# Kernel tuning notes

Measured on AMD Instinct MI355X. Metric: run time of the kernel, lower is better.

The kernel has to match this reference:

```python
import jax, jax.numpy as jnp
import numpy as np

ALPHA = 1.5
TEMPERATURE = 1.0
N_ITER = 25
N_EMBED = 2048
NUM_EXPERTS = 64
N_TOKENS = 32768


def entmax_bisect(X, alpha=ALPHA, n_iter=N_ITER):
    """Faithful port of entmax.entmax_bisect forward (dim=-1)."""
    d = X.shape[-1]
    inv = 1.0 / (alpha - 1.0)
    Xa = X * (alpha - 1.0)
    max_val = jnp.max(Xa, axis=-1, keepdims=True)
    # _gp(1, alpha) = 1 ; _gp(1/d, alpha) = (1/d)**(1/(alpha-1))
    tau_lo = max_val - 1.0
    tau_hi = max_val - (1.0 / d) ** inv

    def p(tau):
        return jnp.clip(Xa - tau, 0.0, None) ** inv

    f_lo = jnp.sum(p(tau_lo), axis=-1, keepdims=True) - 1.0
    dm0 = tau_hi - tau_lo

    def body(carry, _):
        tau_lo, dm = carry
        dm = dm * 0.5
        tau_m = tau_lo + dm
        p_m = p(tau_m)
        f_m = jnp.sum(p_m, axis=-1, keepdims=True) - 1.0
        mask = (f_m * f_lo) >= 0
        tau_lo = jnp.where(mask, tau_m, tau_lo)
        return (tau_lo, dm), tau_m

    (tau_lo, dm), tau_ms = jax.lax.scan(body, (tau_lo, dm0), None, length=n_iter)
    tau_m_last = tau_ms[-1]  # [..., 1] tau used for the returned p_m in torch loop
    p_m = p(tau_m_last)
    # ensure_sum_one
    p_m = p_m / jnp.sum(p_m, axis=-1, keepdims=True)
    return p_m


def setup_inputs() -> dict:
    key = jax.random.key(0)
    kx, kw, kb = jax.random.split(key, 3)
    x = jax.random.normal(kx, (N_TOKENS, N_EMBED), dtype=jnp.float32)
    # nn.Linear default init: U(-1/sqrt(fan_in), 1/sqrt(fan_in))
    bound = 1.0 / np.sqrt(N_EMBED)
    W = jax.random.uniform(kw, (NUM_EXPERTS, N_EMBED), dtype=jnp.float32, minval=-bound, maxval=bound)
    b = jax.random.uniform(kb, (NUM_EXPERTS,), dtype=jnp.float32, minval=-bound, maxval=bound)
    return {"x": x, "W": W, "b": b}


def reference(x, W, b):
    logits = jnp.einsum("td,ed->te", x, W) + b  # [T, E]
    scaled_logits = logits / TEMPERATURE
    return entmax_bisect(scaled_logits)
```

## Files before the change

kernel.cpp:

```cpp
#include <hip/hip_runtime.h>
#include <hip/hip_bf16.h>
#include <stdint.h>

typedef _Float16 half8 __attribute__((ext_vector_type(8)));
typedef float    f32x4 __attribute__((ext_vector_type(4)));

#define N_EMBED   2048
#define N_EXP     64
#define KCHUNK    64
#define NKC       (N_EMBED / KCHUNK)
#define GCH       16
#define TILEB     8192
#define LGT_STRIDE 68
#define LGT_FLOATS (32 * LGT_STRIDE)

__global__ __launch_bounds__(64) void convert_w_kernel(
        const float* __restrict__ W, uint8_t* __restrict__ wsimg) {
    int tid = blockIdx.x * 64 + threadIdx.x;
    int e   = tid >> 8;
    int d0  = (tid & 255) * 8;
    int kc  = d0 >> 6;
    int dd0 = d0 & 63;
    const float* src = W + e * N_EMBED + d0;
    float4 f0 = *(const float4*)(src);
    float4 f1 = *(const float4*)(src + 4);
    float v[8] = {f0.x, f0.y, f0.z, f0.w, f1.x, f1.y, f1.z, f1.w};
    union { _Float16 h[8]; uint4 u; } hv;
#pragma unroll
    for (int j = 0; j < 8; ++j) hv.h[j] = (_Float16)(0.5f * v[j]);
    uint32_t off = (uint32_t)((e * 128 + dd0 * 2) ^ ((e & 7) << 4));
    *(uint4*)(wsimg + (size_t)kc * TILEB + off) = hv.u;
}

__device__ __forceinline__ half8 cvt8(f32x4 p, f32x4 q) {
    half8 h;
    h[0] = (_Float16)p[0]; h[1] = (_Float16)p[1];
    h[2] = (_Float16)p[2]; h[3] = (_Float16)p[3];
    h[4] = (_Float16)q[0]; h[5] = (_Float16)q[1];
    h[6] = (_Float16)q[2]; h[7] = (_Float16)q[3];
    return h;
}

__global__ __launch_bounds__(256, 4) void router_kernel(
        const float* __restrict__ x, const uint8_t* __restrict__ img,
        const float* __restrict__ bias, float* __restrict__ out) {
    __shared__ uint8_t lds[32768];

    const int tid  = threadIdx.x;
    const int wave = tid >> 6;
    const int lane = tid & 63;
    const int l15  = lane & 15;
    const int l4   = lane >> 4;
    const int g    = wave >> 1;
    const int q    = wave & 1;
    const int rowbase = blockIdx.x * 32;
    const float* xrow = x + (size_t)(rowbase + q * 16 + l15) * N_EMBED
                          + g * (GCH * KCHUNK) + l4 * 8;
    uint8_t* gbase = lds + g * 16384;

    uint32_t boff[4][2];
#pragma unroll
    for (int t = 0; t < 4; ++t)
#pragma unroll
        for (int s = 0; s < 2; ++s)
            boff[t][s] = (uint32_t)(((16 * t + l15) * 128 + s * 64 + l4 * 16)
                                    ^ ((l15 & 7) << 4));

    f32x4 acc[4];
#pragma unroll
    for (int t = 0; t < 4; ++t) acc[t] = (f32x4){0.f, 0.f, 0.f, 0.f};

    const int tg = tid >> 7;
    const int t7 = tid & 127;
    auto STAGE2 = [&](int p) {
        const uint8_t* gsrc = img + (size_t)(tg * GCH + 2 * p) * TILEB + t7 * 16;
        uint8_t* dst = lds + tg * 16384 + (p & 1) * 8192 + t7 * 16;
        (void)gsrc; (void)dst;
    };
    (void)STAGE2;
    auto STAGE1 = [&](int kc) {
        const uint8_t* gsrc = img + (size_t)(tg * GCH + kc) * TILEB;
        uint8_t* dst = lds + tg * 16384 + (kc & 1) * 8192;
#pragma unroll
        for (int j = 0; j < 4; ++j) {
            __builtin_amdgcn_global_load_lds(
                (const __attribute__((address_space(1))) void*)(gsrc + j * 2048 + t7 * 16),
                (__attribute__((address_space(3))) void*)(dst + j * 2048 + t7 * 16),
                16, 0, 0);
        }
    };

    f32x4 A0, A1, A2, A3;
    auto LOADA1 = [&](int kc) {
        const float* ap = xrow + kc * KCHUNK;
        A0 = *(const f32x4*)(ap);
        A1 = *(const f32x4*)(ap + 4);
        A2 = *(const f32x4*)(ap + 32);
        A3 = *(const f32x4*)(ap + 36);
    };
    auto MFMAS1 = [&](int kc, half8 a0, half8 a1) {
        const uint8_t* lb = gbase + (size_t)(kc & 1) * 8192;
#pragma unroll
        for (int t = 0; t < 4; ++t) {
            half8 bh = *(const half8*)(lb + boff[t][0]);
            acc[t] = __builtin_amdgcn_mfma_f32_16x16x32_f16(a0, bh, acc[t], 0, 0, 0);
        }
#pragma unroll
        for (int t = 0; t < 4; ++t) {
            half8 bh = *(const half8*)(lb + boff[t][1]);
            acc[t] = __builtin_amdgcn_mfma_f32_16x16x32_f16(a1, bh, acc[t], 0, 0, 0);
        }
    };

    STAGE1(0);
    __builtin_amdgcn_sched_barrier(0);
    LOADA1(0);
    __builtin_amdgcn_sched_barrier(0);
    asm volatile("s_waitcnt vmcnt(4)" ::: "memory");
    __builtin_amdgcn_s_barrier();
    __builtin_amdgcn_sched_barrier(0);

#pragma unroll 1
    for (int kc = 0; kc < GCH - 1; ++kc) {
        STAGE1(kc + 1);
        __builtin_amdgcn_sched_barrier(0);
        {
            half8 a0 = cvt8(A0, A1);
            half8 a1 = cvt8(A2, A3);
            LOADA1(kc + 1);
            MFMAS1(kc, a0, a1);
        }
        asm volatile("s_waitcnt vmcnt(4) lgkmcnt(0)" ::: "memory");
        __builtin_amdgcn_s_barrier();
        __builtin_amdgcn_sched_barrier(0);
    }

    {
        half8 a0 = cvt8(A0, A1);
        half8 a1 = cvt8(A2, A3);
        MFMAS1(GCH - 1, a0, a1);
    }

    __syncthreads();
    {
        float* lgt = (float*)lds + g * LGT_FLOATS;
#pragma unroll
        for (int t = 0; t < 4; ++t)
#pragma unroll
            for (int r = 0; r < 4; ++r)
                lgt[(q * 16 + l4 * 4 + r) * LGT_STRIDE + t * 16 + l15] = acc[t][r];
    }
    __syncthreads();

    const float* L0 = (const float*)lds;
    const float* L1 = L0 + LGT_FLOATS;
    const int row_local = tid >> 3;
    const int eb = (tid & 7) * 8;
    const int base = row_local * LGT_STRIDE + eb;

    float v0, v1, v2, v3, v4, v5, v6, v7;
    {
        float4 u0 = *(const float4*)(L0 + base);
        float4 u1 = *(const float4*)(L0 + base + 4);
        float4 w0 = *(const float4*)(L1 + base);
        float4 w1 = *(const float4*)(L1 + base + 4);
        float4 c0 = *(const float4*)(bias + eb);
        float4 c1 = *(const float4*)(bias + eb + 4);
        v0 = u0.x + w0.x + 0.5f * c0.x;
        v1 = u0.y + w0.y + 0.5f * c0.y;
        v2 = u0.z + w0.z + 0.5f * c0.z;
        v3 = u0.w + w0.w + 0.5f * c0.w;
        v4 = u1.x + w1.x + 0.5f * c1.x;
        v5 = u1.y + w1.y + 0.5f * c1.y;
        v6 = u1.z + w1.z + 0.5f * c1.z;
        v7 = u1.w + w1.w + 0.5f * c1.w;
    }

    float m = fmaxf(fmaxf(fmaxf(v0, v1), fmaxf(v2, v3)),
                    fmaxf(fmaxf(v4, v5), fmaxf(v6, v7)));
    m = fmaxf(m, __shfl_xor(m, 1, 64));
    m = fmaxf(m, __shfl_xor(m, 2, 64));
    m = fmaxf(m, __shfl_xor(m, 4, 64));

    float tau_lo = m - 1.0f;
    float tau_hi = m - 0.000244140625f;
    float dm = tau_hi - tau_lo;

    float s0, d;
    d = fmaxf(v0 - tau_lo, 0.f); s0 = d * d;
    d = fmaxf(v1 - tau_lo, 0.f); s0 = fmaf(d, d, s0);
    d = fmaxf(v2 - tau_lo, 0.f); s0 = fmaf(d, d, s0);
    d = fmaxf(v3 - tau_lo, 0.f); s0 = fmaf(d, d, s0);
    d = fmaxf(v4 - tau_lo, 0.f); s0 = fmaf(d, d, s0);
    d = fmaxf(v5 - tau_lo, 0.f); s0 = fmaf(d, d, s0);
    d = fmaxf(v6 - tau_lo, 0.f); s0 = fmaf(d, d, s0);
    d = fmaxf(v7 - tau_lo, 0.f); s0 = fmaf(d, d, s0);
    s0 += __shfl_xor(s0, 1, 64);
    s0 += __shfl_xor(s0, 2, 64);
    s0 += __shfl_xor(s0, 4, 64);
    const float f_lo = s0 - 1.0f;

    float tau_m = tau_lo, fsum = 1.0f;
#pragma unroll 1
    for (int it = 0; it < 25; ++it) {
        dm *= 0.5f;
        tau_m = tau_lo + dm;
        float s;
        d = fmaxf(v0 - tau_m, 0.f); s = d * d;
        d = fmaxf(v1 - tau_m, 0.f); s = fmaf(d, d, s);
        d = fmaxf(v2 - tau_m, 0.f); s = fmaf(d, d, s);
        d = fmaxf(v3 - tau_m, 0.f); s = fmaf(d, d, s);
        d = fmaxf(v4 - tau_m, 0.f); s = fmaf(d, d, s);
        d = fmaxf(v5 - tau_m, 0.f); s = fmaf(d, d, s);
        d = fmaxf(v6 - tau_m, 0.f); s = fmaf(d, d, s);
        d = fmaxf(v7 - tau_m, 0.f); s = fmaf(d, d, s);
        s += __shfl_xor(s, 1, 64);
        s += __shfl_xor(s, 2, 64);
        s += __shfl_xor(s, 4, 64);
        if ((s - 1.0f) * f_lo >= 0.0f) tau_lo = tau_m;
        fsum = s;
    }
    float rinv = 1.0f / fsum;
    float4 o0, o1;
    d = fmaxf(v0 - tau_m, 0.f); o0.x = d * d * rinv;
    d = fmaxf(v1 - tau_m, 0.f); o0.y = d * d * rinv;
    d = fmaxf(v2 - tau_m, 0.f); o0.z = d * d * rinv;
    d = fmaxf(v3 - tau_m, 0.f); o0.w = d * d * rinv;
    d = fmaxf(v4 - tau_m, 0.f); o1.x = d * d * rinv;
    d = fmaxf(v5 - tau_m, 0.f); o1.y = d * d * rinv;
    d = fmaxf(v6 - tau_m, 0.f); o1.z = d * d * rinv;
    d = fmaxf(v7 - tau_m, 0.f); o1.w = d * d * rinv;

    float* op = out + (size_t)(rowbase + row_local) * N_EXP + eb;
    *(float4*)(op)     = o0;
    *(float4*)(op + 4) = o1;
}

extern "C" void kernel_launch(void* const* d_in, const int* in_sizes, int n_in,
                              void* d_out, int out_size, void* d_ws, size_t ws_size,
                              hipStream_t stream) {
    (void)n_in; (void)out_size; (void)ws_size;
    const float* x  = (const float*)d_in[0];
    const float* W  = (const float*)d_in[1];
    const float* b  = (const float*)d_in[2];
    float* out      = (float*)d_out;
    uint8_t* wsimg  = (uint8_t*)d_ws;

    const int T = in_sizes[0] / N_EMBED;

    convert_w_kernel<<<dim3(256), dim3(64), 0, stream>>>(W, wsimg);
    router_kernel<<<dim3(T / 32), dim3(256), 0, stream>>>(x, wsimg, b, out);
}
```

Before: 66.25 us.

## Load W fragments directly from global in MFMA layout, drop LDS staging, 64-row blocks

```diff
diff --git a/kernel.cpp b/kernel.cpp
--- a/kernel.cpp
+++ b/kernel.cpp
@@ -10,26 +10,25 @@
 #define KCHUNK    64
 #define NKC       (N_EMBED / KCHUNK)
 #define GCH       16
-#define TILEB     8192
 #define LGT_STRIDE 68
-#define LGT_FLOATS (32 * LGT_STRIDE)
+#define LGT_FLOATS (64 * LGT_STRIDE)
 
 __global__ __launch_bounds__(64) void convert_w_kernel(
-        const float* __restrict__ W, uint8_t* __restrict__ wsimg) {
-    int tid = blockIdx.x * 64 + threadIdx.x;
-    int e   = tid >> 8;
-    int d0  = (tid & 255) * 8;
-    int kc  = d0 >> 6;
-    int dd0 = d0 & 63;
-    const float* src = W + e * N_EMBED + d0;
+        const float* __restrict__ W, uint8_t* __restrict__ img) {
+    int tid  = blockIdx.x * 64 + threadIdx.x;
+    int f    = tid >> 6;
+    int lane = tid & 63;
+    int kc = f >> 3, t = (f >> 1) & 3, s = f & 1;
+    int e  = t * 16 + (lane & 15);
+    int d  = kc * 64 + s * 32 + (lane >> 4) * 8;
+    const float* src = W + e * N_EMBED + d;
     float4 f0 = *(const float4*)(src);
     float4 f1 = *(const float4*)(src + 4);
     float v[8] = {f0.x, f0.y, f0.z, f0.w, f1.x, f1.y, f1.z, f1.w};
     union { _Float16 h[8]; uint4 u; } hv;
 #pragma unroll
     for (int j = 0; j < 8; ++j) hv.h[j] = (_Float16)(0.5f * v[j]);
-    uint32_t off = (uint32_t)((e * 128 + dd0 * 2) ^ ((e & 7) << 4));
-    *(uint4*)(wsimg + (size_t)kc * TILEB + off) = hv.u;
+    *(uint4*)(img + (size_t)f * 1024 + lane * 16) = hv.u;
 }
 
 __device__ __forceinline__ half8 cvt8(f32x4 p, f32x4 q) {
@@ -41,104 +40,85 @@
     return h;
 }
 
-__global__ __launch_bounds__(256, 4) void router_kernel(
+__global__ __launch_bounds__(512, 4) void router_kernel(
         const float* __restrict__ x, const uint8_t* __restrict__ img,
         const float* __restrict__ bias, float* __restrict__ out) {
-    __shared__ uint8_t lds[32768];
+    __shared__ uint8_t lds[2 * LGT_FLOATS * 4];
 
     const int tid  = threadIdx.x;
     const int wave = tid >> 6;
     const int lane = tid & 63;
     const int l15  = lane & 15;
     const int l4   = lane >> 4;
-    const int g    = wave >> 1;
-    const int q    = wave & 1;
-    const int rowbase = blockIdx.x * 32;
+    const int g    = wave >> 2;
+    const int q    = wave & 3;
+    const int rowbase = blockIdx.x * 64;
     const float* xrow = x + (size_t)(rowbase + q * 16 + l15) * N_EMBED
                           + g * (GCH * KCHUNK) + l4 * 8;
-    uint8_t* gbase = lds + g * 16384;
-
-    uint32_t boff[4][2];
-#pragma unroll
-    for (int t = 0; t < 4; ++t)
-#pragma unroll
-        for (int s = 0; s < 2; ++s)
-            boff[t][s] = (uint32_t)(((16 * t + l15) * 128 + s * 64 + l4 * 16)
-                                    ^ ((l15 & 7) << 4));
+    const uint8_t* fbase = img + (size_t)g * GCH * 8192 + lane * 16;
 
     f32x4 acc[4];
 #pragma unroll
     for (int t = 0; t < 4; ++t) acc[t] = (f32x4){0.f, 0.f, 0.f, 0.f};
 
-    const int tg = tid >> 7;
-    const int t7 = tid & 127;
-    auto STAGE2 = [&](int p) {
-        const uint8_t* gsrc = img + (size_t)(tg * GCH + 2 * p) * TILEB + t7 * 16;
-        uint8_t* dst = lds + tg * 16384 + (p & 1) * 8192 + t7 * 16;
-        (void)gsrc; (void)dst;
-    };
-    (void)STAGE2;
-    auto STAGE1 = [&](int kc) {
-        const uint8_t* gsrc = img + (size_t)(tg * GCH + kc) * TILEB;
-        uint8_t* dst = lds + tg * 16384 + (kc & 1) * 8192;
-#pragma unroll
-        for (int j = 0; j < 4; ++j) {
-            __builtin_amdgcn_global_load_lds(
-                (const __attribute__((address_space(1))) void*)(gsrc + j * 2048 + t7 * 16),
-                (__attribute__((address_space(3))) void*)(dst + j * 2048 + t7 * 16),
-                16, 0, 0);
-        }
-    };
-
     f32x4 A0, A1, A2, A3;
-    auto LOADA1 = [&](int kc) {
+    auto LOADA = [&](int kc) {
         const float* ap = xrow + kc * KCHUNK;
         A0 = *(const f32x4*)(ap);
         A1 = *(const f32x4*)(ap + 4);
         A2 = *(const f32x4*)(ap + 32);
         A3 = *(const f32x4*)(ap + 36);
     };
-    auto MFMAS1 = [&](int kc, half8 a0, half8 a1) {
-        const uint8_t* lb = gbase + (size_t)(kc & 1) * 8192;
-#pragma unroll
-        for (int t = 0; t < 4; ++t) {
-            half8 bh = *(const half8*)(lb + boff[t][0]);
-            acc[t] = __builtin_amdgcn_mfma_f32_16x16x32_f16(a0, bh, acc[t], 0, 0, 0);
-        }
-#pragma unroll
-        for (int t = 0; t < 4; ++t) {
-            half8 bh = *(const half8*)(lb + boff[t][1]);
-            acc[t] = __builtin_amdgcn_mfma_f32_16x16x32_f16(a1, bh, acc[t], 0, 0, 0);
-        }
+
+    half8 B00, B01, B10, B11, B20, B21, B30, B31;
+    auto LOADB = [&](int kc) {
+        const uint8_t* fb = fbase + (size_t)kc * 8192;
+        B00 = *(const half8*)(fb);
+        B01 = *(const half8*)(fb + 1024);
+        B10 = *(const half8*)(fb + 2048);
+        B11 = *(const half8*)(fb + 3072);
+        B20 = *(const half8*)(fb + 4096);
+        B21 = *(const half8*)(fb + 5120);
+        B30 = *(const half8*)(fb + 6144);
+        B31 = *(const half8*)(fb + 7168);
     };
 
-    STAGE1(0);
-    __builtin_amdgcn_sched_barrier(0);
-    LOADA1(0);
-    __builtin_amdgcn_sched_barrier(0);
-    asm volatile("s_waitcnt vmcnt(4)" ::: "memory");
-    __builtin_amdgcn_s_barrier();
+    LOADA(0);
     __builtin_amdgcn_sched_barrier(0);
 
 #pragma unroll 1
     for (int kc = 0; kc < GCH - 1; ++kc) {
-        STAGE1(kc + 1);
-        __builtin_amdgcn_sched_barrier(0);
-        {
-            half8 a0 = cvt8(A0, A1);
-            half8 a1 = cvt8(A2, A3);
-            LOADA1(kc + 1);
-            MFMAS1(kc, a0, a1);
-        }
-        asm volatile("s_waitcnt vmcnt(4) lgkmcnt(0)" ::: "memory");
-        __builtin_amdgcn_s_barrier();
-        __builtin_amdgcn_sched_barrier(0);
-    }
-
-    {
+        LOADB(kc);
+        __builtin_amdgcn_sched_barrier(0);
         half8 a0 = cvt8(A0, A1);
         half8 a1 = cvt8(A2, A3);
-        MFMAS1(GCH - 1, a0, a1);
+        __builtin_amdgcn_sched_barrier(0);
+        LOADA(kc + 1);
+        __builtin_amdgcn_sched_barrier(0);
+        acc[0] = __builtin_amdgcn_mfma_f32_16x16x32_f16(a0, B00, acc[0], 0, 0, 0);
+        acc[1] = __builtin_amdgcn_mfma_f32_16x16x32_f16(a0, B10, acc[1], 0, 0, 0);
+        acc[2] = __builtin_amdgcn_mfma_f32_16x16x32_f16(a0, B20, acc[2], 0, 0, 0);
+        acc[3] = __builtin_amdgcn_mfma_f32_16x16x32_f16(a0, B30, acc[3], 0, 0, 0);
+        acc[0] = __builtin_amdgcn_mfma_f32_16x16x32_f16(a1, B01, acc[0], 0, 0, 0);
+        acc[1] = __builtin_amdgcn_mfma_f32_16x16x32_f16(a1, B11, acc[1], 0, 0, 0);
+        acc[2] = __builtin_amdgcn_mfma_f32_16x16x32_f16(a1, B21, acc[2], 0, 0, 0);
+        acc[3] = __builtin_amdgcn_mfma_f32_16x16x32_f16(a1, B31, acc[3], 0, 0, 0);
+        __builtin_amdgcn_sched_barrier(0);
+    }
+
+    {
+        LOADB(GCH - 1);
+        __builtin_amdgcn_sched_barrier(0);
+        half8 a0 = cvt8(A0, A1);
+        half8 a1 = cvt8(A2, A3);
+        acc[0] = __builtin_amdgcn_mfma_f32_16x16x32_f16(a0, B00, acc[0], 0, 0, 0);
+        acc[1] = __builtin_amdgcn_mfma_f32_16x16x32_f16(a0, B10, acc[1], 0, 0, 0);
+        acc[2] = __builtin_amdgcn_mfma_f32_16x16x32_f16(a0, B20, acc[2], 0, 0, 0);
+        acc[3] = __builtin_amdgcn_mfma_f32_16x16x32_f16(a0, B30, acc[3], 0, 0, 0);
+        acc[0] = __builtin_amdgcn_mfma_f32_16x16x32_f16(a1, B01, acc[0], 0, 0, 0);
+        acc[1] = __builtin_amdgcn_mfma_f32_16x16x32_f16(a1, B11, acc[1], 0, 0, 0);
+        acc[2] = __builtin_amdgcn_mfma_f32_16x16x32_f16(a1, B21, acc[2], 0, 0, 0);
+        acc[3] = __builtin_amdgcn_mfma_f32_16x16x32_f16(a1, B31, acc[3], 0, 0, 0);
     }
 
     __syncthreads();
@@ -154,8 +134,8 @@
 
     const float* L0 = (const float*)lds;
     const float* L1 = L0 + LGT_FLOATS;
-    const int row_local = tid >> 3;
-    const int eb = (tid & 7) * 8;
+    const int row_local = wave * 8 + (lane >> 3);
+    const int eb = (lane & 7) * 8;
     const int base = row_local * LGT_STRIDE + eb;
 
     float v0, v1, v2, v3, v4, v5, v6, v7;
@@ -249,5 +229,5 @@
     const int T = in_sizes[0] / N_EMBED;
 
     convert_w_kernel<<<dim3(256), dim3(64), 0, stream>>>(W, wsimg);
-    router_kernel<<<dim3(T / 32), dim3(256), 0, stream>>>(x, wsimg, b, out);
-}
+    router_kernel<<<dim3(T / 64), dim3(512), 0, stream>>>(x, wsimg, b, out);
+}
```

Result: no change. 65.54 us (-1.1%).
